# Performance work log

Measured on AMD Instinct MI355X. Metric: run time of the kernel, lower is better.

Reference implementation:

```python
import jax, jax.numpy as jnp
import numpy as np

B, T, N, M = 128, 128, 128, 256  # batch, timesteps, driving series, hidden size


def setup_inputs() -> dict:
    key = jax.random.key(0)
    ks = jax.random.split(key, 8)
    def p(k, shape, fan):
        return jax.random.normal(k, shape, jnp.float32) / np.float32(np.sqrt(fan))
    X = jax.random.normal(ks[0], (B, T, N), jnp.float32)
    h0 = jnp.zeros((B, M), jnp.float32)
    s0 = jnp.zeros((B, M), jnp.float32)
    Wx = p(ks[1], (N, 4 * M), N)           # LSTM input kernel (gates i,f,g,o)
    Wh = p(ks[2], (M, 4 * M), M)           # LSTM recurrent kernel
    b = jnp.zeros((4 * M,), jnp.float32)
    Wd = p(ks[3], (2 * M, T), 2 * M)       # attention W: Dense(T) on [h;s]
    bW = jnp.zeros((T,), jnp.float32)
    Ud = p(ks[4], (T, T), T)               # attention U: Dense(T) on X^T
    bU = jnp.zeros((T,), jnp.float32)
    vd = p(ks[5], (T, 1), T)               # attention v: Dense(1)
    bv = jnp.zeros((1,), jnp.float32)
    return {"X": X, "h0": h0, "s0": s0, "Wx": Wx, "Wh": Wh, "b": b,
            "Wd": Wd, "bW": bW, "Ud": Ud, "bU": bU, "vd": vd, "bv": bv}


def reference(X, h0, s0, Wx, Wh, b, Wd, bW, Ud, bU, vd, bv):
    m = h0.shape[-1]
    # U(Permute(X)) is time-invariant: precompute once. (B,N,T)
    UX = jnp.einsum('btn,tu->bnu', X, Ud) + bU

    def lstm_cell(h, c, x_t):
        z = x_t @ Wx + h @ Wh + b                      # (B,4M)
        i, f, g, o = jnp.split(z, 4, axis=-1)
        i = jax.nn.sigmoid(i)
        f = jax.nn.sigmoid(f)
        g = jnp.tanh(g)
        o = jax.nn.sigmoid(o)
        c = f * c + i * g
        h = o * jnp.tanh(c)
        return h, c

    def step(carry, x_t):
        h, c = carry
        h, c = lstm_cell(h, c, x_t)                    # (B,M),(B,M)
        hs = jnp.concatenate([h, c], axis=-1)          # (B,2M)
        w = hs @ Wd + bW                               # (B,T), broadcast over N
        e = jnp.tanh(w[:, None, :] + UX) @ vd          # (B,N,1)
        alpha = jax.nn.softmax(e[..., 0] + bv[0], axis=-1)  # softmax over N
        return (h, c), alpha

    (_, _), alphas = jax.lax.scan(step, (h0, s0), jnp.swapaxes(X, 0, 1))
    # alphas: (T,B,N) -> (B,T,N); x_tilde = alpha_t (.) x_t
    return X * jnp.swapaxes(alphas, 0, 1)
```

## Files before the change

kernel.cpp:

```cpp
#include <hip/hip_runtime.h>
#include <hip/hip_fp16.h>

#define Bc 128
#define Tc 128
#define Nc 128
#define Mc 256
#define G4 1024

typedef _Float16 half8 __attribute__((ext_vector_type(8)));
typedef float f32x4 __attribute__((ext_vector_type(4)));

__device__ __forceinline__ float frcp(float x) {
#if __has_builtin(__builtin_amdgcn_rcpf)
  return __builtin_amdgcn_rcpf(x);
#else
  return 1.f / x;
#endif
}
__device__ __forceinline__ float fsig(float x) { return frcp(1.f + __expf(-x)); }
__device__ __forceinline__ float ftanh(float x) {
  float t = __expf(2.f * x);
  return 1.f - 2.f * frcp(t + 1.f);
}

__device__ __forceinline__ f32x4 load_x4_cc(const void* p) {
  f32x4 r;
  asm volatile("global_load_dwordx4 %0, %1, off sc0 sc1" : "=v"(r) : "v"(p));
  return r;
}
__device__ __forceinline__ void store_h_cc(void* p, unsigned short v) {
  asm volatile("global_store_short %0, %1, off sc0 sc1" :: "v"(p), "v"((unsigned)v) : "memory");
}

__global__ void k_prep(const float* __restrict__ Wh, const float* __restrict__ h0,
                       __half* __restrict__ wht, __half* __restrict__ hx,
                       unsigned* __restrict__ flags) {
  int bid = blockIdx.x;
  if (bid < 512) {
    int i = bid * 256 + threadIdx.x;
    int jt = i >> 11;
    int rem = i & 2047;
    int kt = rem >> 8;
    int rem2 = rem & 255;
    int lane = rem2 >> 2;
    int r2 = rem2 & 3;
    int jp = jt * 16 + (lane & 15);
    int g = jp & 3, mcol = jp >> 2;
    int j = g * 256 + mcol;
    int mk0 = kt * 32 + (lane >> 4) * 8 + 2 * r2;
    wht[(size_t)i * 2]     = __float2half(Wh[(size_t)mk0 * G4 + j]);
    wht[(size_t)i * 2 + 1] = __float2half(Wh[(size_t)(mk0 + 1) * G4 + j]);
  } else {
    for (int i = threadIdx.x; i < 8 * 4096; i += 256) flags[i] = 0u;
    for (int i = threadIdx.x; i < Bc * Mc; i += 256) hx[i] = __float2half(h0[i]);
  }
}

__global__ void k_ux(const float* __restrict__ X, const float* __restrict__ Ud,
                     const float* __restrict__ bU, float* __restrict__ PX) {
  __shared__ float Xl[Tc][Nc];
  int b = blockIdx.x;
  const float* Xb = X + (size_t)b * Tc * Nc;
  for (int i = threadIdx.x; i < Tc * Nc; i += 256) Xl[i >> 7][i & 127] = Xb[i];
  __syncthreads();
  int n = threadIdx.x & 127;
  int uh = __builtin_amdgcn_readfirstlane(threadIdx.x >> 7);
  for (int u0 = uh * 64; u0 < uh * 64 + 64; u0 += 8) {
    float acc[8];
#pragma unroll
    for (int i = 0; i < 8; i++) acc[i] = 0.f;
    for (int tt = 0; tt < Tc; ++tt) {
      float xv = Xl[tt][n];
#pragma unroll
      for (int i = 0; i < 8; i++) acc[i] += xv * Ud[tt * Tc + u0 + i];
    }
#pragma unroll
    for (int i = 0; i < 8; i++)
      PX[((size_t)b * Tc + (u0 + i)) * Nc + n] = __expf(2.f * (acc[i] + bU[u0 + i]));
  }
}

__global__ __launch_bounds__(256, 2)
void k_xwx2(const float* __restrict__ X, const float* __restrict__ Wx,
            const float* __restrict__ bias, float* __restrict__ XWxP) {
  __shared__ float xl[32][Nc];
  int t = blockIdx.x >> 2;
  int b0 = (blockIdx.x & 3) * 32;
  for (int i = threadIdx.x; i < 32 * Nc; i += 256) {
    int row = i >> 7, n = i & 127;
    xl[row][n] = X[(size_t)(b0 + row) * Tc * Nc + (size_t)t * Nc + n];
  }
  __syncthreads();
  int m = threadIdx.x;
  float acc[32][4];
#pragma unroll
  for (int i = 0; i < 32; i++)
#pragma unroll
    for (int g = 0; g < 4; g++) acc[i][g] = 0.f;
  for (int n = 0; n < Nc; ++n) {
    float wi = Wx[(size_t)n * G4 + m];
    float wf = Wx[(size_t)n * G4 + 256 + m];
    float wg = Wx[(size_t)n * G4 + 512 + m];
    float wo = Wx[(size_t)n * G4 + 768 + m];
#pragma unroll
    for (int i = 0; i < 32; i++) {
      float xv = xl[i][n];
      acc[i][0] += xv * wi; acc[i][1] += xv * wf;
      acc[i][2] += xv * wg; acc[i][3] += xv * wo;
    }
  }
  float bi = bias[m], bf = bias[256 + m], bg = bias[512 + m], bo = bias[768 + m];
#pragma unroll
  for (int i = 0; i < 32; i++) {
    float4 o;
    o.x = acc[i][0] + bi; o.y = acc[i][1] + bf;
    o.z = acc[i][2] + bg; o.w = acc[i][3] + bo;
    *(float4*)(XWxP + ((size_t)t * Bc + b0 + i) * G4 + m * 4) = o;
  }
}

__global__ __launch_bounds__(512, 2)
void k_scan(const __half* __restrict__ wht, const float* __restrict__ xwxp,
            __half* __restrict__ hx, __half* __restrict__ cx,
            unsigned* __restrict__ flags, const float* __restrict__ s0) {
  int bid = blockIdx.x;
  int q = bid >> 3, grp = bid & 7;
  int tid = threadIdx.x;
  int wave = tid >> 6, lane = tid & 63;
  int lb = lane & 15, lg = lane >> 4;
  int b = grp * 16 + lb;
  int jt0 = q * 16 + wave * 2;

  half8 A[2][8];
#pragma unroll
  for (int u = 0; u < 2; ++u)
#pragma unroll
    for (int kt = 0; kt < 8; ++kt)
      A[u][kt] = *(const half8*)(wht + ((size_t)((jt0 + u) * 8 + kt) * 64 + lane) * 8);

  int m0 = jt0 * 4 + lg;
  float c0 = s0[(size_t)b * Mc + m0];
  float c1 = s0[(size_t)b * Mc + m0 + 4];

  unsigned* flg = flags + grp * 4096;

  for (int t = 0; t < 128; ++t) {
    const float* xp = xwxp + ((size_t)t * Bc + b) * G4 + lg * 4;
    f32x4 acc0 = *(const f32x4*)(xp + (size_t)jt0 * 16);
    f32x4 acc1 = *(const f32x4*)(xp + (size_t)(jt0 + 1) * 16);

    if (t > 0 && lane == 0) {
      while (__hip_atomic_load(flg + t * 16, __ATOMIC_RELAXED,
                               __HIP_MEMORY_SCOPE_AGENT) < 4u) {}
    }
    const __half* hxt = hx + (size_t)t * (Bc * Mc) + (size_t)b * Mc + lg * 8;
    f32x4 braw[8];
#pragma unroll
    for (int kt = 0; kt < 8; ++kt)
      braw[kt] = load_x4_cc(hxt + kt * 32);
    asm volatile("s_waitcnt vmcnt(0)" ::: "memory");
    __builtin_amdgcn_sched_barrier(0);

#pragma unroll
    for (int kt = 0; kt < 8; ++kt) {
      half8 Bf = __builtin_bit_cast(half8, braw[kt]);
      acc0 = __builtin_amdgcn_mfma_f32_16x16x32_f16(A[0][kt], Bf, acc0, 0, 0, 0);
      acc1 = __builtin_amdgcn_mfma_f32_16x16x32_f16(A[1][kt], Bf, acc1, 0, 0, 0);
    }
    float i0 = fsig(acc0[0]), f0 = fsig(acc0[1]);
    float g0 = ftanh(acc0[2]), o0 = fsig(acc0[3]);
    c0 = f0 * c0 + i0 * g0;
    float h0v = o0 * ftanh(c0);
    float i1 = fsig(acc1[0]), f1 = fsig(acc1[1]);
    float g1 = ftanh(acc1[2]), o1 = fsig(acc1[3]);
    c1 = f1 * c1 + i1 * g1;
    float h1v = o1 * ftanh(c1);

    __half* hob = hx + (size_t)(t + 1) * (Bc * Mc) + (size_t)b * Mc;
    store_h_cc(hob + m0,     __half_as_ushort(__float2half(h0v)));
    store_h_cc(hob + m0 + 4, __half_as_ushort(__float2half(h1v)));
    asm volatile("s_waitcnt vmcnt(0)" ::: "memory");
    __syncthreads();
    if (tid == 0)
      __hip_atomic_fetch_add(flg + (t + 1) * 16, 1u, __ATOMIC_RELAXED,
                             __HIP_MEMORY_SCOPE_AGENT);
    __half* cob = cx + (size_t)t * (Bc * Mc) + (size_t)b * Mc;
    cob[m0]     = __float2half(c0);
    cob[m0 + 4] = __float2half(c1);
  }
}

__global__ void k_wall2(const __half2* __restrict__ Hx2, const __half2* __restrict__ Cx2,
                        const float* __restrict__ Wd, const float* __restrict__ bW,
                        float* __restrict__ Wall) {
  int r0 = blockIdx.x * 32;
  int wv = __builtin_amdgcn_readfirstlane(threadIdx.x >> 6);
  int lane = threadIdx.x & 63;
  int u2 = lane * 2;
  int rbase = r0 + wv * 8;
  float acc[8][2];
#pragma unroll
  for (int i = 0; i < 8; i++) { acc[i][0] = 0.f; acc[i][1] = 0.f; }
#pragma unroll 2
  for (int k2 = 0; k2 < 128; ++k2) {
    float2 wh0 = *(const float2*)(Wd + (size_t)(2 * k2) * Tc + u2);
    float2 wh1 = *(const float2*)(Wd + (size_t)(2 * k2 + 1) * Tc + u2);
    float2 wc0 = *(const float2*)(Wd + (size_t)(Mc + 2 * k2) * Tc + u2);
    float2 wc1 = *(const float2*)(Wd + (size_t)(Mc + 2 * k2 + 1) * Tc + u2);
#pragma unroll
    for (int i = 0; i < 8; i++) {
      __half2 hv = Hx2[(size_t)(rbase + i) * 128 + 16384 + k2];
      __half2 cv = Cx2[(size_t)(rbase + i) * 128 + k2];
      float hlo = __low2float(hv), hhi = __high2float(hv);
      float clo = __low2float(cv), chi = __high2float(cv);
      acc[i][0] += hlo * wh0.x + hhi * wh1.x + clo * wc0.x + chi * wc1.x;
      acc[i][1] += hlo * wh0.y + hhi * wh1.y + clo * wc0.y + chi * wc1.y;
    }
  }
  float bw0 = bW[u2], bw1 = bW[u2 + 1];
#pragma unroll
  for (int i = 0; i < 8; i++) {
    float2 o; o.x = acc[i][0] + bw0; o.y = acc[i][1] + bw1;
    *(float2*)(Wall + (size_t)(rbase + i) * Tc + u2) = o;
  }
}

__global__ void k_attn(const float* __restrict__ Wall, const float* __restrict__ PX,
                       const float* __restrict__ vd, const float* __restrict__ X,
                       float* __restrict__ out) {
  __shared__ float4 av[Nc];
  __shared__ float v2s[Nc];
  __shared__ float wred[2][4];
  int b = blockIdx.x & 127, tq = blockIdx.x >> 7;
  int n = threadIdx.x;
  int wv = n >> 6;
  float4 a;
  a.x = __expf(2.f * Wall[((size_t)(tq * 4 + 0) * Bc + b) * Tc + n]);
  a.y = __expf(2.f * Wall[((size_t)(tq * 4 + 1) * Bc + b) * Tc + n]);
  a.z = __expf(2.f * Wall[((size_t)(tq * 4 + 2) * Bc + b) * Tc + n]);
  a.w = __expf(2.f * Wall[((size_t)(tq * 4 + 3) * Bc + b) * Tc + n]);
  av[n] = a;
  v2s[n] = -2.f * vd[n];
  __syncthreads();
  const float* Pb = PX + (size_t)b * Tc * Nc;
  float e0 = 0.f, e1 = 0.f, e2 = 0.f, e3 = 0.f;
#pragma unroll 4
  for (int u = 0; u < Tc; ++u) {
    float P = Pb[(size_t)u * Nc + n];
    float4 au = av[u];
    float v2 = v2s[u];
    e0 = fmaf(v2, frcp(fmaf(au.x, P, 1.f)), e0);
    e1 = fmaf(v2, frcp(fmaf(au.y, P, 1.f)), e1);
    e2 = fmaf(v2, frcp(fmaf(au.z, P, 1.f)), e2);
    e3 = fmaf(v2, frcp(fmaf(au.w, P, 1.f)), e3);
  }
  float e[4] = {e0, e1, e2, e3};
  float M[4], S[4], ex[4];
#pragma unroll
  for (int k = 0; k < 4; ++k) {
    float m = e[k];
#pragma unroll
    for (int off = 32; off > 0; off >>= 1) m = fmaxf(m, __shfl_xor(m, off));
    if ((n & 63) == 0) wred[wv][k] = m;
  }
  __syncthreads();
#pragma unroll
  for (int k = 0; k < 4; ++k) M[k] = fmaxf(wred[0][k], wred[1][k]);
  __syncthreads();
#pragma unroll
  for (int k = 0; k < 4; ++k) {
    ex[k] = __expf(e[k] - M[k]);
    float s = ex[k];
#pragma unroll
    for (int off = 32; off > 0; off >>= 1) s += __shfl_xor(s, off);
    if ((n & 63) == 0) wred[wv][k] = s;
  }
  __syncthreads();
#pragma unroll
  for (int k = 0; k < 4; ++k) S[k] = wred[0][k] + wred[1][k];
#pragma unroll
  for (int k = 0; k < 4; ++k) {
    int t = tq * 4 + k;
    size_t xi = ((size_t)b * Tc + t) * Nc + n;
    out[xi] = X[xi] * (ex[k] * frcp(S[k]));
  }
}

extern "C" void kernel_launch(void* const* d_in, const int* in_sizes, int n_in,
                              void* d_out, int out_size, void* d_ws, size_t ws_size,
                              hipStream_t stream) {
  (void)in_sizes; (void)n_in; (void)out_size; (void)ws_size;
  const float* X  = (const float*)d_in[0];
  const float* h0 = (const float*)d_in[1];
  const float* s0 = (const float*)d_in[2];
  const float* Wx = (const float*)d_in[3];
  const float* Wh = (const float*)d_in[4];
  const float* bb = (const float*)d_in[5];
  const float* Wd = (const float*)d_in[6];
  const float* bW = (const float*)d_in[7];
  const float* Ud = (const float*)d_in[8];
  const float* bU = (const float*)d_in[9];
  const float* vd = (const float*)d_in[10];
  float* out = (float*)d_out;
  float* ws = (float*)d_ws;

  float* PX   = ws;
  float* XWxP = PX + 2097152;
  __half* hx  = (__half*)(XWxP + 16777216);
  __half* cx  = hx + 129 * 32768;
  float* Wall = (float*)(cx + 128 * 32768);
  __half* wht = (__half*)(Wall + 2097152);
  unsigned* flags = (unsigned*)(wht + 262144);

  k_prep<<<513, 256, 0, stream>>>(Wh, h0, wht, hx, flags);
  k_ux<<<Bc, 256, 0, stream>>>(X, Ud, bU, PX);
  k_xwx2<<<Tc * 4, 256, 0, stream>>>(X, Wx, bb, XWxP);
  k_scan<<<32, 512, 0, stream>>>(wht, XWxP, hx, cx, flags, s0);
  k_wall2<<<(Tc * Bc) / 32, 256, 0, stream>>>((const __half2*)hx, (const __half2*)cx,
                                              Wd, bW, Wall);
  k_attn<<<Bc * 32, 128, 0, stream>>>(Wall, PX, vd, X, out);
}
```

Baseline: 713.6 us.

## Restructure LSTM scan: per-wave byte flags, 4 batch groups per block, software prefetch

The recurrent scan kernel now runs 8 blocks instead of 32, and each block interleaves 4 batch groups of 16. While one group computes, the next group's h, x-projection and flag loads are already in flight. The shared per-block atomic counter with __syncthreads is replaced by per-wave byte flags, which consumers poll as packed dwordx4 words, so no block-wide barrier is needed each step. This is meant to hide global-memory and cross-block synchronisation latency on the serial critical path. In exchange it uses fewer CUs, relies on hand-written inline asm waitcnt counts, and polls with a busy spin, all of which are fragile.

```diff
diff --git a/kernel.cpp b/kernel.cpp
--- a/kernel.cpp
+++ b/kernel.cpp
@@ -9,6 +9,7 @@
 
 typedef _Float16 half8 __attribute__((ext_vector_type(8)));
 typedef float f32x4 __attribute__((ext_vector_type(4)));
+typedef unsigned u32x4 __attribute__((ext_vector_type(4)));
 
 __device__ __forceinline__ float frcp(float x) {
 #if __has_builtin(__builtin_amdgcn_rcpf)
@@ -23,14 +24,23 @@
   return 1.f - 2.f * frcp(t + 1.f);
 }
 
-__device__ __forceinline__ f32x4 load_x4_cc(const void* p) {
-  f32x4 r;
-  asm volatile("global_load_dwordx4 %0, %1, off sc0 sc1" : "=v"(r) : "v"(p));
-  return r;
-}
-__device__ __forceinline__ void store_h_cc(void* p, unsigned short v) {
-  asm volatile("global_store_short %0, %1, off sc0 sc1" :: "v"(p), "v"((unsigned)v) : "memory");
-}
+#define LDX4CC(dst, ptr, OFF) \
+  asm volatile("global_load_dwordx4 %0, %1, off offset:" #OFF " sc0 sc1" \
+               : "=&v"(dst) : "v"(ptr))
+#define LDX4P(dst, ptr, OFF) \
+  asm volatile("global_load_dwordx4 %0, %1, off offset:" #OFF \
+               : "=&v"(dst) : "v"(ptr))
+#define STHCC(ptr, v_, OFF) \
+  asm volatile("global_store_short %0, %1, off offset:" #OFF " sc0 sc1" \
+               :: "v"(ptr), "v"(v_))
+#define STHP(ptr, v_, OFF) \
+  asm volatile("global_store_short %0, %1, off offset:" #OFF \
+               :: "v"(ptr), "v"(v_))
+#define STBCC(ptr, v_, OFF) \
+  asm volatile("global_store_byte %0, %1, off offset:" #OFF " sc0 sc1" \
+               :: "v"(ptr), "v"(v_))
+#define VMCNT(N) do { asm volatile("s_waitcnt vmcnt(" #N ")" ::: "memory"); \
+                      __builtin_amdgcn_sched_barrier(0); } while (0)
 
 __global__ void k_prep(const float* __restrict__ Wh, const float* __restrict__ h0,
                        __half* __restrict__ wht, __half* __restrict__ hx,
@@ -119,17 +129,66 @@
   }
 }
 
+#define SLOT(G, GN, PO0, PO1, CO0, CO1, FOFF, X3) \
+  { \
+    constexpr int cb_ = (G) & 1, nb_ = ((G) + 1) & 1; \
+    const char* hB_ = hp[GN] + ((X3) ? 65536 : 0); \
+    const char* xB_ = xp[GN] + ((X3) ? xadv : 0); \
+    asm volatile("global_load_dwordx4 %0, %2, off offset:" #PO0 " sc0 sc1\n\t" \
+                 "global_load_dwordx4 %1, %2, off offset:" #PO1 " sc0 sc1" \
+                 : "=&v"(pv[nb_][0]), "=&v"(pv[nb_][1]) : "v"(dp)); \
+    LDX4CC(hbuf[nb_][0], hB_, 0);   LDX4CC(hbuf[nb_][1], hB_, 64); \
+    LDX4CC(hbuf[nb_][2], hB_, 128); LDX4CC(hbuf[nb_][3], hB_, 192); \
+    LDX4CC(hbuf[nb_][4], hB_, 256); LDX4CC(hbuf[nb_][5], hB_, 320); \
+    LDX4CC(hbuf[nb_][6], hB_, 384); LDX4CC(hbuf[nb_][7], hB_, 448); \
+    LDX4P(xbuf[nb_][0], xB_, 0);    LDX4P(xbuf[nb_][1], xB_, 64); \
+    if ((G) == 0 && t == 0) { VMCNT(12); } else { VMCNT(17); } \
+    if (t > 0) { \
+      u32x4 pa_ = pv[cb_][0], pb_ = pv[cb_][1]; \
+      while ((pa_.x & pa_.y & pa_.z & pa_.w & pb_.x & pb_.y & pb_.z & pb_.w) \
+             != 0x01010101u) { \
+        asm volatile("global_load_dwordx4 %0, %2, off offset:" #CO0 " sc0 sc1\n\t" \
+                     "global_load_dwordx4 %1, %2, off offset:" #CO1 " sc0 sc1\n\t" \
+                     "s_waitcnt vmcnt(0)" \
+                     : "=&v"(pa_), "=&v"(pb_) : "v"(dp) : "memory"); \
+      } \
+    } \
+    if (lane == 0) STBCC(fp, onev, FOFF); \
+    f32x4 acc0_ = xbuf[cb_][0], acc1_ = xbuf[cb_][1]; \
+    _Pragma("unroll") \
+    for (int kt = 0; kt < 8; ++kt) { \
+      half8 Bf_ = __builtin_bit_cast(half8, hbuf[cb_][kt]); \
+      acc0_ = __builtin_amdgcn_mfma_f32_16x16x32_f16(A[0][kt], Bf_, acc0_, 0, 0, 0); \
+      acc1_ = __builtin_amdgcn_mfma_f32_16x16x32_f16(A[1][kt], Bf_, acc1_, 0, 0, 0); \
+    } \
+    float i0_ = fsig(acc0_[0]), f0_ = fsig(acc0_[1]); \
+    float g0_ = ftanh(acc0_[2]), o0_ = fsig(acc0_[3]); \
+    c0g[G] = f0_ * c0g[G] + i0_ * g0_; \
+    float h0_ = o0_ * ftanh(c0g[G]); \
+    float i1_ = fsig(acc1_[0]), f1_ = fsig(acc1_[1]); \
+    float g1_ = ftanh(acc1_[2]), o1_ = fsig(acc1_[3]); \
+    c1g[G] = f1_ * c1g[G] + i1_ * g1_; \
+    float h1_ = o1_ * ftanh(c1g[G]); \
+    char* hs_ = (char*)hp[G] + hsoff; \
+    STHCC(hs_, (unsigned)__half_as_ushort(__float2half(h0_)), 0); \
+    STHCC(hs_, (unsigned)__half_as_ushort(__float2half(h1_)), 8); \
+    char* cs_ = hs_ + cdel; \
+    STHP(cs_, (unsigned)__half_as_ushort(__float2half(c0g[G])), 0); \
+    STHP(cs_, (unsigned)__half_as_ushort(__float2half(c1g[G])), 8); \
+  }
+
 __global__ __launch_bounds__(512, 2)
 void k_scan(const __half* __restrict__ wht, const float* __restrict__ xwxp,
             __half* __restrict__ hx, __half* __restrict__ cx,
             unsigned* __restrict__ flags, const float* __restrict__ s0) {
   int bid = blockIdx.x;
-  int q = bid >> 3, grp = bid & 7;
+  int set = bid >> 2, q = bid & 3;
   int tid = threadIdx.x;
-  int wave = tid >> 6, lane = tid & 63;
+  int wave = __builtin_amdgcn_readfirstlane(tid >> 6);
+  int lane = tid & 63;
   int lb = lane & 15, lg = lane >> 4;
-  int b = grp * 16 + lb;
   int jt0 = q * 16 + wave * 2;
+  int m0 = jt0 * 4 + lg;
 
   half8 A[2][8];
 #pragma unroll
@@ -138,55 +197,48 @@
     for (int kt = 0; kt < 8; ++kt)
       A[u][kt] = *(const half8*)(wht + ((size_t)((jt0 + u) * 8 + kt) * 64 + lane) * 8);
 
-  int m0 = jt0 * 4 + lg;
-  float c0 = s0[(size_t)b * Mc + m0];
-  float c1 = s0[(size_t)b * Mc + m0 + 4];
-
-  unsigned* flg = flags + grp * 4096;
-
+  float c0g[4], c1g[4];
+  const char* hp[4];
+  const char* xp[4];
+#pragma unroll
+  for (int g = 0; g < 4; ++g) {
+    int bg = set * 64 + g * 16 + lb;
+    c0g[g] = s0[(size_t)bg * Mc + m0];
+    c1g[g] = s0[(size_t)bg * Mc + m0 + 4];
+    hp[g] = (const char*)hx + (size_t)(bg * Mc + lg * 8) * 2;
+    xp[g] = (const char*)xwxp + (size_t)(bg * G4 + jt0 * 16 + lg * 4) * 4;
+  }
+  const char* dp = (const char*)flags + set * 16512;
+  char* fp = (char*)flags + set * 16512 + q * 8 + wave;
+  const int hsoff = 65536 + (jt0 * 4 - 7 * lg) * 2;
+  const ptrdiff_t cdel = (const char*)cx - (const char*)hx - 65536;
+  unsigned onev = 1u;
+
+  f32x4 hbuf[2][8];
+  f32x4 xbuf[2][2];
+  u32x4 pv[2][2];
+
+  asm volatile("s_waitcnt vmcnt(0)" ::: "memory");
+  __builtin_amdgcn_sched_barrier(0);
+  asm volatile("global_load_dwordx4 %0, %2, off offset:0 sc0 sc1\n\t"
+               "global_load_dwordx4 %1, %2, off offset:16 sc0 sc1"
+               : "=&v"(pv[0][0]), "=&v"(pv[0][1]) : "v"(dp));
+  LDX4CC(hbuf[0][0], hp[0], 0);   LDX4CC(hbuf[0][1], hp[0], 64);
+  LDX4CC(hbuf[0][2], hp[0], 128); LDX4CC(hbuf[0][3], hp[0], 192);
+  LDX4CC(hbuf[0][4], hp[0], 256); LDX4CC(hbuf[0][5], hp[0], 320);
+  LDX4CC(hbuf[0][6], hp[0], 384); LDX4CC(hbuf[0][7], hp[0], 448);
+  LDX4P(xbuf[0][0], xp[0], 0);    LDX4P(xbuf[0][1], xp[0], 64);
+
+#pragma unroll 1
   for (int t = 0; t < 128; ++t) {
-    const float* xp = xwxp + ((size_t)t * Bc + b) * G4 + lg * 4;
-    f32x4 acc0 = *(const f32x4*)(xp + (size_t)jt0 * 16);
-    f32x4 acc1 = *(const f32x4*)(xp + (size_t)(jt0 + 1) * 16);
-
-    if (t > 0 && lane == 0) {
-      while (__hip_atomic_load(flg + t * 16, __ATOMIC_RELAXED,
-                               __HIP_MEMORY_SCOPE_AGENT) < 4u) {}
-    }
-    const __half* hxt = hx + (size_t)t * (Bc * Mc) + (size_t)b * Mc + lg * 8;
-    f32x4 braw[8];
-#pragma unroll
-    for (int kt = 0; kt < 8; ++kt)
-      braw[kt] = load_x4_cc(hxt + kt * 32);
-    asm volatile("s_waitcnt vmcnt(0)" ::: "memory");
-    __builtin_amdgcn_sched_barrier(0);
-
-#pragma unroll
-    for (int kt = 0; kt < 8; ++kt) {
-      half8 Bf = __builtin_bit_cast(half8, braw[kt]);
-      acc0 = __builtin_amdgcn_mfma_f32_16x16x32_f16(A[0][kt], Bf, acc0, 0, 0, 0);
-      acc1 = __builtin_amdgcn_mfma_f32_16x16x32_f16(A[1][kt], Bf, acc1, 0, 0, 0);
-    }
-    float i0 = fsig(acc0[0]), f0 = fsig(acc0[1]);
-    float g0 = ftanh(acc0[2]), o0 = fsig(acc0[3]);
-    c0 = f0 * c0 + i0 * g0;
-    float h0v = o0 * ftanh(c0);
-    float i1 = fsig(acc1[0]), f1 = fsig(acc1[1]);
-    float g1 = ftanh(acc1[2]), o1 = fsig(acc1[3]);
-    c1 = f1 * c1 + i1 * g1;
-    float h1v = o1 * ftanh(c1);
-
-    __half* hob = hx + (size_t)(t + 1) * (Bc * Mc) + (size_t)b * Mc;
-    store_h_cc(hob + m0,     __half_as_ushort(__float2half(h0v)));
-    store_h_cc(hob + m0 + 4, __half_as_ushort(__float2half(h1v)));
-    asm volatile("s_waitcnt vmcnt(0)" ::: "memory");
-    __syncthreads();
-    if (tid == 0)
-      __hip_atomic_fetch_add(flg + (t + 1) * 16, 1u, __ATOMIC_RELAXED,
-                             __HIP_MEMORY_SCOPE_AGENT);
-    __half* cob = cx + (size_t)t * (Bc * Mc) + (size_t)b * Mc;
-    cob[m0]     = __float2half(c0);
-    cob[m0 + 4] = __float2half(c1);
+    const long xadv = (t < 127) ? 524288 : 0;
+    SLOT(0, 1,  32,  48,   0,  16,  64, 0)
+    SLOT(1, 2,  64,  80,  32,  48,  96, 0)
+    SLOT(2, 3,  96, 112,  64,  80, 128, 0)
+    SLOT(3, 0, 128, 144,  96, 112, 160, 1)
+    hp[0] += 65536; hp[1] += 65536; hp[2] += 65536; hp[3] += 65536;
+    xp[0] += 524288; xp[1] += 524288; xp[2] += 524288; xp[3] += 524288;
+    dp += 128; fp += 128;
   }
 }
 
@@ -315,7 +367,7 @@
   k_prep<<<513, 256, 0, stream>>>(Wh, h0, wht, hx, flags);
   k_ux<<<Bc, 256, 0, stream>>>(X, Ud, bU, PX);
   k_xwx2<<<Tc * 4, 256, 0, stream>>>(X, Wx, bb, XWxP);
-  k_scan<<<32, 512, 0, stream>>>(wht, XWxP, hx, cx, flags, s0);
+  k_scan<<<8, 512, 0, stream>>>(wht, XWxP, hx, cx, flags, s0);
   k_wall2<<<(Tc * Bc) / 32, 256, 0, stream>>>((const __half2*)hx, (const __half2*)cx,
                                               Wd, bW, Wall);
   k_attn<<<Bc * 32, 128, 0, stream>>>(Wall, PX, vd, X, out);
```

Result: slower. 2.225 ms (+211.8%).

## Replace flag-counter barrier with inverted-sentinel data polling in LSTM scan

Applied to the files above, without the earlier changes.

The per-step synchronisation in the recurrent scan no longer uses an atomic counter plus a block-wide barrier. Each hidden value is stored bitwise-inverted, packed as two fp16 values per dword, into a zero-initialised buffer, and consumers spin-reload the h vector until no dword is zero. This removes the syncthreads and the atomic round trip from the critical path of the recurrence. The Wh fragment layout and the attention projection indexing are permuted to match the new pairing. The cost is that k_prep must zero the whole h history buffer, and every lane re-polls the full vector. Correctness relies on an inverted packed value never being zero, which only fails if both halves are the fp16 bit pattern 0xFFFF (a NaN).

```diff
diff --git a/kernel.cpp b/kernel.cpp
--- a/kernel.cpp
+++ b/kernel.cpp
@@ -9,6 +9,7 @@
 
 typedef _Float16 half8 __attribute__((ext_vector_type(8)));
 typedef float f32x4 __attribute__((ext_vector_type(4)));
+typedef unsigned u32x4 __attribute__((ext_vector_type(4)));
 
 __device__ __forceinline__ float frcp(float x) {
 #if __has_builtin(__builtin_amdgcn_rcpf)
@@ -23,18 +24,16 @@
   return 1.f - 2.f * frcp(t + 1.f);
 }
 
-__device__ __forceinline__ f32x4 load_x4_cc(const void* p) {
-  f32x4 r;
-  asm volatile("global_load_dwordx4 %0, %1, off sc0 sc1" : "=v"(r) : "v"(p));
-  return r;
-}
-__device__ __forceinline__ void store_h_cc(void* p, unsigned short v) {
-  asm volatile("global_store_short %0, %1, off sc0 sc1" :: "v"(p), "v"((unsigned)v) : "memory");
-}
+#define LDX4CC(dst, ptr, OFF) \
+  asm volatile("global_load_dwordx4 %0, %1, off offset:" #OFF " sc0 sc1" \
+               : "=v"(dst) : "v"(ptr))
+#define STDWCC(ptr, v_) \
+  asm volatile("global_store_dword %0, %1, off sc0 sc1" :: "v"(ptr), "v"(v_))
+#define VMCNT0 do { asm volatile("s_waitcnt vmcnt(0)" ::: "memory"); \
+                    __builtin_amdgcn_sched_barrier(0); } while (0)
 
 __global__ void k_prep(const float* __restrict__ Wh, const float* __restrict__ h0,
-                       __half* __restrict__ wht, __half* __restrict__ hx,
-                       unsigned* __restrict__ flags) {
+                       __half* __restrict__ wht, unsigned* __restrict__ hx2) {
   int bid = blockIdx.x;
   if (bid < 512) {
     int i = bid * 256 + threadIdx.x;
@@ -47,12 +46,19 @@
     int jp = jt * 16 + (lane & 15);
     int g = jp & 3, mcol = jp >> 2;
     int j = g * 256 + mcol;
-    int mk0 = kt * 32 + (lane >> 4) * 8 + 2 * r2;
+    int mk0 = kt * 32 + (lane >> 4) * 8 + r2;
     wht[(size_t)i * 2]     = __float2half(Wh[(size_t)mk0 * G4 + j]);
-    wht[(size_t)i * 2 + 1] = __float2half(Wh[(size_t)(mk0 + 1) * G4 + j]);
+    wht[(size_t)i * 2 + 1] = __float2half(Wh[(size_t)(mk0 + 4) * G4 + j]);
+  } else if (bid < 576) {
+    int idx = (bid - 512) * 256 + threadIdx.x;
+    int b = idx >> 7, i = idx & 127;
+    int a = i >> 2, d = i & 3;
+    unsigned lo = __half_as_ushort(__float2half(h0[(size_t)b * Mc + 8 * a + d]));
+    unsigned hi = __half_as_ushort(__float2half(h0[(size_t)b * Mc + 8 * a + d + 4]));
+    hx2[idx] = ~(lo | (hi << 16));
   } else {
-    for (int i = threadIdx.x; i < 8 * 4096; i += 256) flags[i] = 0u;
-    for (int i = threadIdx.x; i < Bc * Mc; i += 256) hx[i] = __float2half(h0[i]);
+    int idx = (bid - 576) * 256 + threadIdx.x;
+    hx2[16384 + idx] = 0u;
   }
 }
 
@@ -119,17 +125,19 @@
   }
 }
 
-__global__ __launch_bounds__(512, 2)
+__global__ __launch_bounds__(512, 1)
 void k_scan(const __half* __restrict__ wht, const float* __restrict__ xwxp,
-            __half* __restrict__ hx, __half* __restrict__ cx,
-            unsigned* __restrict__ flags, const float* __restrict__ s0) {
+            unsigned* __restrict__ hx2, __half* __restrict__ cx,
+            const float* __restrict__ s0) {
   int bid = blockIdx.x;
   int q = bid >> 3, grp = bid & 7;
   int tid = threadIdx.x;
-  int wave = tid >> 6, lane = tid & 63;
+  int wave = __builtin_amdgcn_readfirstlane(tid >> 6);
+  int lane = tid & 63;
   int lb = lane & 15, lg = lane >> 4;
   int b = grp * 16 + lb;
   int jt0 = q * 16 + wave * 2;
+  int m0 = jt0 * 4 + lg;
 
   half8 A[2][8];
 #pragma unroll
@@ -138,32 +146,44 @@
     for (int kt = 0; kt < 8; ++kt)
       A[u][kt] = *(const half8*)(wht + ((size_t)((jt0 + u) * 8 + kt) * 64 + lane) * 8);
 
-  int m0 = jt0 * 4 + lg;
   float c0 = s0[(size_t)b * Mc + m0];
   float c1 = s0[(size_t)b * Mc + m0 + 4];
 
-  unsigned* flg = flags + grp * 4096;
-
+  const char* hq = (const char*)hx2 + ((size_t)b * 128 + lg * 4) * 4;
+  char*       hs = (char*)hx2 + ((size_t)16384 + b * 128 + jt0 * 2 + lg) * 4;
+  const float* xq = xwxp + ((size_t)b) * G4 + jt0 * 16 + lg * 4;
+  __half*      cq = cx + (size_t)b * Mc;
+
+  f32x4 braw[8];
+
+#pragma unroll 1
   for (int t = 0; t < 128; ++t) {
-    const float* xp = xwxp + ((size_t)t * Bc + b) * G4 + lg * 4;
-    f32x4 acc0 = *(const f32x4*)(xp + (size_t)jt0 * 16);
-    f32x4 acc1 = *(const f32x4*)(xp + (size_t)(jt0 + 1) * 16);
-
-    if (t > 0 && lane == 0) {
-      while (__hip_atomic_load(flg + t * 16, __ATOMIC_RELAXED,
-                               __HIP_MEMORY_SCOPE_AGENT) < 4u) {}
-    }
-    const __half* hxt = hx + (size_t)t * (Bc * Mc) + (size_t)b * Mc + lg * 8;
-    f32x4 braw[8];
-#pragma unroll
-    for (int kt = 0; kt < 8; ++kt)
-      braw[kt] = load_x4_cc(hxt + kt * 32);
-    asm volatile("s_waitcnt vmcnt(0)" ::: "memory");
-    __builtin_amdgcn_sched_barrier(0);
+    f32x4 acc0 = *(const f32x4*)(xq);
+    f32x4 acc1 = *(const f32x4*)(xq + 16);
+
+    LDX4CC(braw[0], hq, 0);   LDX4CC(braw[1], hq, 64);
+    LDX4CC(braw[2], hq, 128); LDX4CC(braw[3], hq, 192);
+    LDX4CC(braw[4], hq, 256); LDX4CC(braw[5], hq, 320);
+    LDX4CC(braw[6], hq, 384); LDX4CC(braw[7], hq, 448);
+    for (;;) {
+      VMCNT0;
+      unsigned mn = 0xFFFFFFFFu;
+#pragma unroll
+      for (int kt = 0; kt < 8; ++kt) {
+        u32x4 u = __builtin_bit_cast(u32x4, braw[kt]);
+        mn = min(mn, min(min(u.x, u.y), min(u.z, u.w)));
+      }
+      if (__builtin_expect(mn != 0u, 1)) break;
+      LDX4CC(braw[0], hq, 0);   LDX4CC(braw[1], hq, 64);
+      LDX4CC(braw[2], hq, 128); LDX4CC(braw[3], hq, 192);
+      LDX4CC(braw[4], hq, 256); LDX4CC(braw[5], hq, 320);
+      LDX4CC(braw[6], hq, 384); LDX4CC(braw[7], hq, 448);
+    }
 
 #pragma unroll
     for (int kt = 0; kt < 8; ++kt) {
-      half8 Bf = __builtin_bit_cast(half8, braw[kt]);
+      u32x4 u = ~__builtin_bit_cast(u32x4, braw[kt]);
+      half8 Bf = __builtin_bit_cast(half8, u);
       acc0 = __builtin_amdgcn_mfma_f32_16x16x32_f16(A[0][kt], Bf, acc0, 0, 0, 0);
       acc1 = __builtin_amdgcn_mfma_f32_16x16x32_f16(A[1][kt], Bf, acc1, 0, 0, 0);
     }
@@ -176,21 +196,18 @@
     c1 = f1 * c1 + i1 * g1;
     float h1v = o1 * ftanh(c1);
 
-    __half* hob = hx + (size_t)(t + 1) * (Bc * Mc) + (size_t)b * Mc;
-    store_h_cc(hob + m0,     __half_as_ushort(__float2half(h0v)));
-    store_h_cc(hob + m0 + 4, __half_as_ushort(__float2half(h1v)));
-    asm volatile("s_waitcnt vmcnt(0)" ::: "memory");
-    __syncthreads();
-    if (tid == 0)
-      __hip_atomic_fetch_add(flg + (t + 1) * 16, 1u, __ATOMIC_RELAXED,
-                             __HIP_MEMORY_SCOPE_AGENT);
-    __half* cob = cx + (size_t)t * (Bc * Mc) + (size_t)b * Mc;
-    cob[m0]     = __float2half(c0);
-    cob[m0 + 4] = __float2half(c1);
-  }
-}
-
-__global__ void k_wall2(const __half2* __restrict__ Hx2, const __half2* __restrict__ Cx2,
+    unsigned pk = (unsigned)__half_as_ushort(__float2half(h0v)) |
+                  ((unsigned)__half_as_ushort(__float2half(h1v)) << 16);
+    STDWCC(hs, ~pk);
+
+    cq[m0]     = __float2half(c0);
+    cq[m0 + 4] = __float2half(c1);
+
+    hq += 65536; hs += 65536; xq += Bc * G4; cq += Bc * Mc;
+  }
+}
+
+__global__ void k_wall2(const unsigned* __restrict__ Hxu, const __half2* __restrict__ Cx2,
                         const float* __restrict__ Wd, const float* __restrict__ bW,
                         float* __restrict__ Wall) {
   int r0 = blockIdx.x * 32;
@@ -203,13 +220,15 @@
   for (int i = 0; i < 8; i++) { acc[i][0] = 0.f; acc[i][1] = 0.f; }
 #pragma unroll 2
   for (int k2 = 0; k2 < 128; ++k2) {
-    float2 wh0 = *(const float2*)(Wd + (size_t)(2 * k2) * Tc + u2);
-    float2 wh1 = *(const float2*)(Wd + (size_t)(2 * k2 + 1) * Tc + u2);
+    int m_lo = 8 * (k2 >> 2) + (k2 & 3);
+    float2 wh0 = *(const float2*)(Wd + (size_t)m_lo * Tc + u2);
+    float2 wh1 = *(const float2*)(Wd + (size_t)(m_lo + 4) * Tc + u2);
     float2 wc0 = *(const float2*)(Wd + (size_t)(Mc + 2 * k2) * Tc + u2);
     float2 wc1 = *(const float2*)(Wd + (size_t)(Mc + 2 * k2 + 1) * Tc + u2);
 #pragma unroll
     for (int i = 0; i < 8; i++) {
-      __half2 hv = Hx2[(size_t)(rbase + i) * 128 + 16384 + k2];
+      unsigned hraw = ~Hxu[(size_t)(rbase + i) * 128 + 16384 + k2];
+      __half2 hv = __builtin_bit_cast(__half2, hraw);
       __half2 cv = Cx2[(size_t)(rbase + i) * 128 + k2];
       float hlo = __low2float(hv), hhi = __high2float(hv);
       float clo = __low2float(cv), chi = __high2float(cv);
@@ -304,19 +323,17 @@
   float* out = (float*)d_out;
   float* ws = (float*)d_ws;
 
-  float* PX   = ws;
-  float* XWxP = PX + 2097152;
-  __half* hx  = (__half*)(XWxP + 16777216);
-  __half* cx  = hx + 129 * 32768;
-  float* Wall = (float*)(cx + 128 * 32768);
-  __half* wht = (__half*)(Wall + 2097152);
-  unsigned* flags = (unsigned*)(wht + 262144);
-
-  k_prep<<<513, 256, 0, stream>>>(Wh, h0, wht, hx, flags);
+  float* PX       = ws;
+  float* XWxP     = PX + 2097152;
+  unsigned* hx2   = (unsigned*)(XWxP + 16777216);
+  __half* cx      = (__half*)(hx2 + 129 * 16384);
+  float* Wall     = (float*)(cx + 128 * 32768);
+  __half* wht     = (__half*)(Wall + 2097152);
+
+  k_prep<<<8768, 256, 0, stream>>>(Wh, h0, wht, hx2);
   k_ux<<<Bc, 256, 0, stream>>>(X, Ud, bU, PX);
   k_xwx2<<<Tc * 4, 256, 0, stream>>>(X, Wx, bb, XWxP);
-  k_scan<<<32, 512, 0, stream>>>(wht, XWxP, hx, cx, flags, s0);
-  k_wall2<<<(Tc * Bc) / 32, 256, 0, stream>>>((const __half2*)hx, (const __half2*)cx,
-                                              Wd, bW, Wall);
+  k_scan<<<32, 512, 0, stream>>>(wht, XWxP, hx2, cx, s0);
+  k_wall2<<<(Tc * Bc) / 32, 256, 0, stream>>>(hx2, (const __half2*)cx, Wd, bW, Wall);
   k_attn<<<Bc * 32, 128, 0, stream>>>(Wall, PX, vd, X, out);
 }
```

New measurement: 931.0 us. 1.3x slower.
